# Kernel optimization log

Hardware: AMD Instinct MI355X
Metric: run time of the kernel (lower is better)

## Reference

```python
import jax, jax.numpy as jnp
import numpy as np

B, T, D, V, E = 128, 256, 1024, 32000, 300


def setup_inputs() -> dict:
    key = jax.random.key(0)
    ks = jax.random.split(key, 9)
    s = lambda d: 1.0 / np.sqrt(d)
    return {
        "input_to_decoder": jax.random.randint(ks[0], (B, 1), 0, V),
        "encoder_output": jax.random.normal(ks[1], (B, T, D), jnp.float32) * s(D),
        "state_h": jax.random.normal(ks[2], (B, D), jnp.float32) * s(D),
        "state_c": jax.random.normal(ks[3], (B, D), jnp.float32) * s(D),
        "emb_table": jax.random.normal(ks[4], (V, E), jnp.float32) * 0.02,
        "W_lstm": jax.random.normal(ks[5], (D + E, 4 * D), jnp.float32) * s(D + E),
        "U_lstm": jax.random.normal(ks[6], (D, 4 * D), jnp.float32) * s(D),
        "b_lstm": jnp.zeros((4 * D,), jnp.float32),
        "W_dense": jax.random.normal(ks[7], (D, V), jnp.float32) * s(D),
        "b_dense": jnp.zeros((V,), jnp.float32),
    }


def reference(input_to_decoder, encoder_output, state_h, state_c,
              emb_table, W_lstm, U_lstm, b_lstm, W_dense, b_dense):
    # embedding lookup + squeeze(axis=1): [B,1] -> [B,E]
    emb = emb_table[input_to_decoder[:, 0]]
    # Bahdanau-style dot scores: [B,T]
    scores = jnp.einsum("btd,bd->bt", encoder_output, state_h)
    # NOTE: faithful to source - context uses RAW (pre-softmax) scores
    context = jnp.einsum("btd,bt->bd", encoder_output, scores)  # [B,D]
    attention_weights = jax.nn.softmax(scores, axis=1)[..., None]  # [B,T,1]
    # concat context + embedding, single LSTM cell step (Keras gate order i,f,g,o)
    x = jnp.concatenate([context, emb], axis=1)  # [B,D+E]
    z = x @ W_lstm + state_h @ U_lstm + b_lstm  # [B,4D]
    zi, zf, zg, zo = jnp.split(z, 4, axis=1)
    c_new = jax.nn.sigmoid(zf) * state_c + jax.nn.sigmoid(zi) * jnp.tanh(zg)
    h_new = jax.nn.sigmoid(zo) * jnp.tanh(c_new)
    logits = h_new @ W_dense + b_dense  # [B,V]
    return logits, h_new, c_new, attention_weights, context
```

## Files before the change

### kernel.cpp

```cpp
#include <hip/hip_runtime.h>
#include <hip/hip_bf16.h>
#include <cmath>


#define Bc 128
#define Tc 256
#define Dc 1024
#define Vc 32000
#define Ec 300
#define KREAL 2348
#define KXP 2688
#define KSPLIT 7
#define N4 4096

typedef __attribute__((ext_vector_type(8))) short bf16x8;
typedef __attribute__((ext_vector_type(4))) float f32x4;

static __device__ __forceinline__ short f2bf(float x) {
    __hip_bfloat16 b = __float2bfloat16(x);
    return *reinterpret_cast<short*>(&b);
}
static __device__ __forceinline__ unsigned pack2(float a, float b) {
    return (unsigned)(unsigned short)f2bf(a) | ((unsigned)(unsigned short)f2bf(b) << 16);
}

__global__ __launch_bounds__(1024) void k_att(
        const float* __restrict__ enc, const float* __restrict__ h,
        const int* __restrict__ idx, const float* __restrict__ emb_table,
        float* __restrict__ ctx_out, float* __restrict__ attn_out,
        unsigned short* __restrict__ x_bf) {
    const int b = blockIdx.x;
    const int tid = threadIdx.x;
    const int wave = tid >> 6, lane = tid & 63;
    __shared__ float s_acc[16][1024];
    __shared__ float s_sc[256];
    __shared__ float red[256];

    const float4* h4 = (const float4*)(h + ((size_t)b << 10));
    float4 hv0 = h4[lane], hv1 = h4[lane + 64], hv2 = h4[lane + 128], hv3 = h4[lane + 192];

    float4 a0 = {0,0,0,0}, a1 = {0,0,0,0}, a2 = {0,0,0,0}, a3 = {0,0,0,0};
    const int t0 = wave << 4;
    const float4* e4 = (const float4*)(enc + ((size_t)(b * Tc + t0) << 10));

    #pragma unroll 2
    for (int i = 0; i < 16; ++i) {
        float4 e0 = e4[lane], e1 = e4[lane + 64], e2 = e4[lane + 128], e3 = e4[lane + 192];
        e4 += 256;
        float d = e0.x*hv0.x + e0.y*hv0.y + e0.z*hv0.z + e0.w*hv0.w
                + e1.x*hv1.x + e1.y*hv1.y + e1.z*hv1.z + e1.w*hv1.w
                + e2.x*hv2.x + e2.y*hv2.y + e2.z*hv2.z + e2.w*hv2.w
                + e3.x*hv3.x + e3.y*hv3.y + e3.z*hv3.z + e3.w*hv3.w;
        #pragma unroll
        for (int off = 32; off; off >>= 1) d += __shfl_xor(d, off, 64);
        if (lane == 0) s_sc[t0 + i] = d;
        a0.x += d*e0.x; a0.y += d*e0.y; a0.z += d*e0.z; a0.w += d*e0.w;
        a1.x += d*e1.x; a1.y += d*e1.y; a1.z += d*e1.z; a1.w += d*e1.w;
        a2.x += d*e2.x; a2.y += d*e2.y; a2.z += d*e2.z; a2.w += d*e2.w;
        a3.x += d*e3.x; a3.y += d*e3.y; a3.z += d*e3.z; a3.w += d*e3.w;
    }
    *(float4*)&s_acc[wave][lane << 2]         = a0;
    *(float4*)&s_acc[wave][256 + (lane << 2)] = a1;
    *(float4*)&s_acc[wave][512 + (lane << 2)] = a2;
    *(float4*)&s_acc[wave][768 + (lane << 2)] = a3;
    __syncthreads();

    float cv = 0.f;
    #pragma unroll
    for (int w = 0; w < 16; ++w) cv += s_acc[w][tid];
    ctx_out[((size_t)b << 10) + tid] = cv;
    s_acc[0][tid] = cv;
    __syncthreads();

    unsigned short* xb = x_bf + (size_t)b * KXP;
    if (tid < 512) {
        *(unsigned*)&xb[tid << 1] = pack2(s_acc[0][tid << 1], s_acc[0][(tid << 1) + 1]);
        float2 hp = *(const float2*)(h + ((size_t)b << 10) + (tid << 1));
        *(unsigned*)&xb[(Dc + Ec) + (tid << 1)] = pack2(hp.x, hp.y);
    } else if (tid < 812) {
        int i = tid - 512;
        int row = idx[b];
        xb[Dc + i] = (unsigned short)f2bf(emb_table[(size_t)row * Ec + i]);
    } else if (tid < 812 + (KXP - KREAL)) {
        xb[KREAL + (tid - 812)] = 0;
    }

    float v = (tid < 256) ? s_sc[tid] : -1e30f;
    if (tid < 256) red[tid] = v;
    __syncthreads();
    for (int s = 128; s; s >>= 1) {
        if (tid < s) red[tid] = fmaxf(red[tid], red[tid + s]);
        __syncthreads();
    }
    float m = red[0];
    __syncthreads();
    float e = __expf(v - m);
    if (tid < 256) red[tid] = e;
    __syncthreads();
    for (int s = 128; s; s >>= 1) {
        if (tid < s) red[tid] += red[tid + s];
        __syncthreads();
    }
    if (tid < 256) attn_out[(b << 8) + tid] = e / red[0];
}

__global__ __launch_bounds__(512) void k_zgemm_mfma(
        const unsigned short* __restrict__ xbf, const float* __restrict__ Wl,
        const float* __restrict__ Ul, float* __restrict__ z_part) {
    __shared__ __align__(16) short blds[2 * 8 * 64 * 8];
    const int tid  = threadIdx.x;
    const int wid  = tid >> 6;
    const int lane = tid & 63;
    const int g    = lane >> 4;
    const int r    = lane & 15;
    const int n0   = blockIdx.x << 6;
    const int ksp  = blockIdx.y;

    const int pr = tid >> 4;
    const int c  = tid & 15;
    const int kk = (pr << 1) & 31;
    const int gg = kk >> 3, jj = kk & 7;
    const int ks0 = pr >> 4;

    f32x4 acc[4] = {};
    const unsigned short* xrow = xbf + (size_t)((wid << 4) + r) * KXP;

    float4 wra[2], wrb[2];
    bf16x8 areg[2][2];

    auto loadWU = [&](int gk) -> float4 {
        if (gk < 1324) return *(const float4*)(Wl + (size_t)gk * N4 + n0 + (c << 2));
        if (gk < KREAL) return *(const float4*)(Ul + (size_t)(gk - 1324) * N4 + n0 + (c << 2));
        return float4{0.f, 0.f, 0.f, 0.f};
    };

    {
        const int kt = (ksp * 6) << 6;
        wra[0] = loadWU(kt + (pr << 1));
        wrb[0] = loadWU(kt + (pr << 1) + 1);
        areg[0][0] = *(const bf16x8*)&xrow[kt + (g << 3)];
        areg[0][1] = *(const bf16x8*)&xrow[kt + 32 + (g << 3)];
    }

    #pragma unroll
    for (int t = 0; t < 6; ++t) {
        const int cur = t & 1;
        const int coff = cur << 12;
        {
            const float av[4] = {wra[cur].x, wra[cur].y, wra[cur].z, wra[cur].w};
            const float bv[4] = {wrb[cur].x, wrb[cur].y, wrb[cur].z, wrb[cur].w};
            #pragma unroll
            for (int i = 0; i < 4; ++i) {
                int n = (c << 2) + i;
                int nt = n >> 4;
                int inner = (gg << 4) | (n & 15);
                int Xs = ((((ks0 << 2) + nt) << 6) | inner) ^ nt;
                *(unsigned*)&blds[coff + (Xs << 3) + jj] = pack2(av[i], bv[i]);
            }
        }
        if (t < 5) {
            const int kt = ((ksp * 6) + t + 1) << 6;
            wra[cur ^ 1] = loadWU(kt + (pr << 1));
            wrb[cur ^ 1] = loadWU(kt + (pr << 1) + 1);
            areg[cur ^ 1][0] = *(const bf16x8*)&xrow[kt + (g << 3)];
            areg[cur ^ 1][1] = *(const bf16x8*)&xrow[kt + 32 + (g << 3)];
        }
        __syncthreads();
        #pragma unroll
        for (int ks = 0; ks < 2; ++ks) {
            #pragma unroll
            for (int nt = 0; nt < 4; ++nt) {
                int Xs = ((((ks << 2) + nt) << 6) | lane) ^ nt;
                bf16x8 bfr = *(const bf16x8*)&blds[coff + (Xs << 3)];
                acc[nt] = __builtin_amdgcn_mfma_f32_16x16x32_bf16(areg[cur][ks], bfr, acc[nt], 0, 0, 0);
            }
        }
    }

    float* zp = z_part + ((size_t)ksp << 19);
    #pragma unroll
    for (int nt = 0; nt < 4; ++nt) {
        int col = n0 + (nt << 4) + r;
        #pragma unroll
        for (int j = 0; j < 4; ++j) {
            int rowm = (wid << 4) + (g << 2) + j;
            zp[((size_t)rowm << 12) + col] = acc[nt][j];
        }
    }
}

__global__ void k_gates(const float* __restrict__ z_part, const float* __restrict__ b_lstm,
                        const float* __restrict__ c_in, float* __restrict__ h_new,
                        float* __restrict__ c_new, unsigned short* __restrict__ h_bf) {
    int i = blockIdx.x * 256 + threadIdx.x;
    int b = i >> 8, d4 = (i & 255) << 2;
    size_t base = ((size_t)b << 12) + d4;
    float4 zi = *(const float4*)(b_lstm + d4);
    float4 zf = *(const float4*)(b_lstm + d4 + 1024);
    float4 zg = *(const float4*)(b_lstm + d4 + 2048);
    float4 zo = *(const float4*)(b_lstm + d4 + 3072);
    #pragma unroll
    for (int ks = 0; ks < KSPLIT; ++ks) {
        const float* zp = z_part + ((size_t)ks << 19);
        float4 t;
        t = *(const float4*)(zp + base);        zi.x += t.x; zi.y += t.y; zi.z += t.z; zi.w += t.w;
        t = *(const float4*)(zp + base + 1024); zf.x += t.x; zf.y += t.y; zf.z += t.z; zf.w += t.w;
        t = *(const float4*)(zp + base + 2048); zg.x += t.x; zg.y += t.y; zg.z += t.z; zg.w += t.w;
        t = *(const float4*)(zp + base + 3072); zo.x += t.x; zo.y += t.y; zo.z += t.z; zo.w += t.w;
    }
    float4 cin = *(const float4*)(c_in + ((size_t)b << 10) + d4);
    float4 cn, hn;
    {
        float si = 1.f/(1.f+__expf(-zi.x)), sf = 1.f/(1.f+__expf(-zf.x)), so = 1.f/(1.f+__expf(-zo.x));
        cn.x = sf*cin.x + si*tanhf(zg.x); hn.x = so*tanhf(cn.x);
        si = 1.f/(1.f+__expf(-zi.y)); sf = 1.f/(1.f+__expf(-zf.y)); so = 1.f/(1.f+__expf(-zo.y));
        cn.y = sf*cin.y + si*tanhf(zg.y); hn.y = so*tanhf(cn.y);
        si = 1.f/(1.f+__expf(-zi.z)); sf = 1.f/(1.f+__expf(-zf.z)); so = 1.f/(1.f+__expf(-zo.z));
        cn.z = sf*cin.z + si*tanhf(zg.z); hn.z = so*tanhf(cn.z);
        si = 1.f/(1.f+__expf(-zi.w)); sf = 1.f/(1.f+__expf(-zf.w)); so = 1.f/(1.f+__expf(-zo.w));
        cn.w = sf*cin.w + si*tanhf(zg.w); hn.w = so*tanhf(cn.w);
    }
    *(float4*)(c_new + ((size_t)b << 10) + d4) = cn;
    *(float4*)(h_new + ((size_t)b << 10) + d4) = hn;
    uint2 hp; hp.x = pack2(hn.x, hn.y); hp.y = pack2(hn.z, hn.w);
    *(uint2*)&h_bf[((size_t)b << 10) + d4] = hp;
}

__global__ __launch_bounds__(512) void k_logits_mfma(
        const unsigned short* __restrict__ hbf, const float* __restrict__ Wd,
        const float* __restrict__ bd, float* __restrict__ out) {
    __shared__ __align__(16) short blds[2 * 16 * 64 * 8];
    const int tid  = threadIdx.x;
    const int wid  = tid >> 6;
    const int lane = tid & 63;
    const int g    = lane >> 4;
    const int r    = lane & 15;
    const int n0   = blockIdx.x << 6;

    const int pr = tid >> 4;
    const int c  = tid & 15;
    const int kk = (pr << 1) & 31;
    const int gg = kk >> 3, jj = kk & 7;
    const int ksA = pr >> 4;
    const int ksB = ksA + 2;

    f32x4 acc[4] = {};
    const unsigned short* hrow = hbf + ((size_t)((wid << 4) + r) << 10);
    const float* wbase = Wd + (size_t)(pr << 1) * Vc + n0 + (c << 2);

    float4 wra[2], wrb[2], wrc[2], wrd[2];
    bf16x8 areg[2][4];

    {
        wra[0] = *(const float4*)(wbase);
        wrb[0] = *(const float4*)(wbase + Vc);
        wrc[0] = *(const float4*)(wbase + (size_t)64 * Vc);
        wrd[0] = *(const float4*)(wbase + (size_t)65 * Vc);
        #pragma unroll
        for (int ks = 0; ks < 4; ++ks)
            areg[0][ks] = *(const bf16x8*)&hrow[(ks << 5) + (g << 3)];
    }

    #pragma unroll
    for (int t = 0; t < 8; ++t) {
        const int cur = t & 1;
        const int coff = cur << 13;
        {
            const float a0[4] = {wra[cur].x, wra[cur].y, wra[cur].z, wra[cur].w};
            const float b0[4] = {wrb[cur].x, wrb[cur].y, wrb[cur].z, wrb[cur].w};
            const float c0[4] = {wrc[cur].x, wrc[cur].y, wrc[cur].z, wrc[cur].w};
            const float d0[4] = {wrd[cur].x, wrd[cur].y, wrd[cur].z, wrd[cur].w};
            #pragma unroll
            for (int i = 0; i < 4; ++i) {
                int n = (c << 2) + i;
                int nt = n >> 4;
                int inner = (gg << 4) | (n & 15);
                int XsA = ((((ksA << 2) + nt) << 6) | inner) ^ nt;
                int XsB = ((((ksB << 2) + nt) << 6) | inner) ^ nt;
                *(unsigned*)&blds[coff + (XsA << 3) + jj] = pack2(a0[i], b0[i]);
                *(unsigned*)&blds[coff + (XsB << 3) + jj] = pack2(c0[i], d0[i]);
            }
        }
        if (t < 7) {
            const float* wb2 = wbase + (size_t)((t + 1) << 7) * Vc;
            wra[cur ^ 1] = *(const float4*)(wb2);
            wrb[cur ^ 1] = *(const float4*)(wb2 + Vc);
            wrc[cur ^ 1] = *(const float4*)(wb2 + (size_t)64 * Vc);
            wrd[cur ^ 1] = *(const float4*)(wb2 + (size_t)65 * Vc);
            #pragma unroll
            for (int ks = 0; ks < 4; ++ks)
                areg[cur ^ 1][ks] = *(const bf16x8*)&hrow[((t + 1) << 7) + (ks << 5) + (g << 3)];
        }
        __syncthreads();
        #pragma unroll
        for (int ks = 0; ks < 4; ++ks) {
            #pragma unroll
            for (int nt = 0; nt < 4; ++nt) {
                int Xs = ((((ks << 2) + nt) << 6) | lane) ^ nt;
                bf16x8 bfr = *(const bf16x8*)&blds[coff + (Xs << 3)];
                acc[nt] = __builtin_amdgcn_mfma_f32_16x16x32_bf16(areg[cur][ks], bfr, acc[nt], 0, 0, 0);
            }
        }
    }

    #pragma unroll
    for (int nt = 0; nt < 4; ++nt) {
        int col = n0 + (nt << 4) + r;
        float bias = bd[col];
        #pragma unroll
        for (int j = 0; j < 4; ++j) {
            int row = (wid << 4) + (g << 2) + j;
            out[(size_t)row * Vc + col] = acc[nt][j] + bias;
        }
    }
}

extern "C" void kernel_launch(void* const* d_in, const int* in_sizes, int n_in,
                              void* d_out, int out_size, void* d_ws, size_t ws_size,
                              hipStream_t stream) {
    const int*   idx = (const int*)d_in[0];
    const float* enc = (const float*)d_in[1];
    const float* h   = (const float*)d_in[2];
    const float* c   = (const float*)d_in[3];
    const float* emb = (const float*)d_in[4];
    const float* Wl  = (const float*)d_in[5];
    const float* Ul  = (const float*)d_in[6];
    const float* bl  = (const float*)d_in[7];
    const float* Wd  = (const float*)d_in[8];
    const float* bd  = (const float*)d_in[9];

    float* out    = (float*)d_out;
    float* logits = out;
    float* h_new  = out + 4096000;
    float* c_new  = out + 4227072;
    float* attn   = out + 4358144;
    float* ctx    = out + 4390912;

    float*          z_part = out;
    unsigned short* x_bf16 = (unsigned short*)d_ws;
    unsigned short* h_bf16 = (unsigned short*)d_ws + 344064;

    hipLaunchKernelGGL(k_att, dim3(128), dim3(1024), 0, stream, enc, h, idx, emb, ctx, attn, x_bf16);
    hipLaunchKernelGGL(k_zgemm_mfma, dim3(64, KSPLIT), dim3(512), 0, stream, x_bf16, Wl, Ul, z_part);
    hipLaunchKernelGGL(k_gates, dim3(128), dim3(256), 0, stream, z_part, bl, c, h_new, c_new, h_bf16);
    hipLaunchKernelGGL(k_logits_mfma, dim3(500), dim3(512), 0, stream, h_bf16, Wd, bd, logits);
}
```

Before: 92.23 us.

## Fuse all stages into one cooperative persistent kernel with grid syncs

```diff
diff --git a/kernel.cpp b/kernel.cpp
--- a/kernel.cpp
+++ b/kernel.cpp
@@ -1,6 +1,9 @@
 #include <hip/hip_runtime.h>
 #include <hip/hip_bf16.h>
+#include <hip/hip_cooperative_groups.h>
 #include <cmath>
+
+namespace cg = cooperative_groups;
 
 
 #define Bc 128
@@ -24,293 +27,310 @@
     return (unsigned)(unsigned short)f2bf(a) | ((unsigned)(unsigned short)f2bf(b) << 16);
 }
 
-__global__ __launch_bounds__(1024) void k_att(
+__global__ __launch_bounds__(512, 2) void k_mega(
         const float* __restrict__ enc, const float* __restrict__ h,
         const int* __restrict__ idx, const float* __restrict__ emb_table,
-        float* __restrict__ ctx_out, float* __restrict__ attn_out,
-        unsigned short* __restrict__ x_bf) {
-    const int b = blockIdx.x;
-    const int tid = threadIdx.x;
-    const int wave = tid >> 6, lane = tid & 63;
-    __shared__ float s_acc[16][1024];
-    __shared__ float s_sc[256];
-    __shared__ float red[256];
-
-    const float4* h4 = (const float4*)(h + ((size_t)b << 10));
-    float4 hv0 = h4[lane], hv1 = h4[lane + 64], hv2 = h4[lane + 128], hv3 = h4[lane + 192];
-
-    float4 a0 = {0,0,0,0}, a1 = {0,0,0,0}, a2 = {0,0,0,0}, a3 = {0,0,0,0};
-    const int t0 = wave << 4;
-    const float4* e4 = (const float4*)(enc + ((size_t)(b * Tc + t0) << 10));
-
-    #pragma unroll 2
-    for (int i = 0; i < 16; ++i) {
-        float4 e0 = e4[lane], e1 = e4[lane + 64], e2 = e4[lane + 128], e3 = e4[lane + 192];
-        e4 += 256;
-        float d = e0.x*hv0.x + e0.y*hv0.y + e0.z*hv0.z + e0.w*hv0.w
-                + e1.x*hv1.x + e1.y*hv1.y + e1.z*hv1.z + e1.w*hv1.w
-                + e2.x*hv2.x + e2.y*hv2.y + e2.z*hv2.z + e2.w*hv2.w
-                + e3.x*hv3.x + e3.y*hv3.y + e3.z*hv3.z + e3.w*hv3.w;
+        const float* __restrict__ Wl, const float* __restrict__ Ul,
+        const float* __restrict__ bl, const float* __restrict__ c_in,
+        const float* __restrict__ Wd, const float* __restrict__ bd,
+        float* __restrict__ logits, float* __restrict__ h_new,
+        float* __restrict__ c_new, float* __restrict__ attn,
+        float* __restrict__ ctx_out,
+        float* __restrict__ ctx_part, float* __restrict__ scores_g,
+        float* __restrict__ z_part,
+        unsigned short* __restrict__ x_bf, unsigned short* __restrict__ h_bf) {
+    cg::grid_group grid = cg::this_grid();
+    __shared__ __align__(16) char smem[32768];
+    const int tid  = threadIdx.x;
+    const int wave = tid >> 6;
+    const int lane = tid & 63;
+
+    {
+        const int tc = blockIdx.x >> 7;
+        const int b  = blockIdx.x & 127;
+        float (*s_acc)[1024] = (float (*)[1024])smem;
+
+        const float4* h4 = (const float4*)(h + ((size_t)b << 10));
+        float4 hv0 = h4[lane], hv1 = h4[lane + 64], hv2 = h4[lane + 128], hv3 = h4[lane + 192];
+
+        float4 a0 = {0,0,0,0}, a1 = {0,0,0,0}, a2 = {0,0,0,0}, a3 = {0,0,0,0};
+        const int t0 = (tc << 7) + (wave << 4);
+        const float4* e4 = (const float4*)(enc + ((size_t)(b * Tc + t0) << 10));
+
+        #pragma unroll 2
+        for (int i = 0; i < 16; ++i) {
+            float4 e0 = e4[lane], e1 = e4[lane + 64], e2 = e4[lane + 128], e3 = e4[lane + 192];
+            e4 += 256;
+            float d = e0.x*hv0.x + e0.y*hv0.y + e0.z*hv0.z + e0.w*hv0.w
+                    + e1.x*hv1.x + e1.y*hv1.y + e1.z*hv1.z + e1.w*hv1.w
+                    + e2.x*hv2.x + e2.y*hv2.y + e2.z*hv2.z + e2.w*hv2.w
+                    + e3.x*hv3.x + e3.y*hv3.y + e3.z*hv3.z + e3.w*hv3.w;
+            #pragma unroll
+            for (int off = 32; off; off >>= 1) d += __shfl_xor(d, off, 64);
+            if (lane == 0) scores_g[(b << 8) + t0 + i] = d;
+            a0.x += d*e0.x; a0.y += d*e0.y; a0.z += d*e0.z; a0.w += d*e0.w;
+            a1.x += d*e1.x; a1.y += d*e1.y; a1.z += d*e1.z; a1.w += d*e1.w;
+            a2.x += d*e2.x; a2.y += d*e2.y; a2.z += d*e2.z; a2.w += d*e2.w;
+            a3.x += d*e3.x; a3.y += d*e3.y; a3.z += d*e3.z; a3.w += d*e3.w;
+        }
+        *(float4*)&s_acc[wave][lane << 2]         = a0;
+        *(float4*)&s_acc[wave][256 + (lane << 2)] = a1;
+        *(float4*)&s_acc[wave][512 + (lane << 2)] = a2;
+        *(float4*)&s_acc[wave][768 + (lane << 2)] = a3;
+        __syncthreads();
         #pragma unroll
-        for (int off = 32; off; off >>= 1) d += __shfl_xor(d, off, 64);
-        if (lane == 0) s_sc[t0 + i] = d;
-        a0.x += d*e0.x; a0.y += d*e0.y; a0.z += d*e0.z; a0.w += d*e0.w;
-        a1.x += d*e1.x; a1.y += d*e1.y; a1.z += d*e1.z; a1.w += d*e1.w;
-        a2.x += d*e2.x; a2.y += d*e2.y; a2.z += d*e2.z; a2.w += d*e2.w;
-        a3.x += d*e3.x; a3.y += d*e3.y; a3.z += d*e3.z; a3.w += d*e3.w;
-    }
-    *(float4*)&s_acc[wave][lane << 2]         = a0;
-    *(float4*)&s_acc[wave][256 + (lane << 2)] = a1;
-    *(float4*)&s_acc[wave][512 + (lane << 2)] = a2;
-    *(float4*)&s_acc[wave][768 + (lane << 2)] = a3;
-    __syncthreads();
-
-    float cv = 0.f;
-    #pragma unroll
-    for (int w = 0; w < 16; ++w) cv += s_acc[w][tid];
-    ctx_out[((size_t)b << 10) + tid] = cv;
-    s_acc[0][tid] = cv;
-    __syncthreads();
-
-    unsigned short* xb = x_bf + (size_t)b * KXP;
-    if (tid < 512) {
-        *(unsigned*)&xb[tid << 1] = pack2(s_acc[0][tid << 1], s_acc[0][(tid << 1) + 1]);
-        float2 hp = *(const float2*)(h + ((size_t)b << 10) + (tid << 1));
-        *(unsigned*)&xb[(Dc + Ec) + (tid << 1)] = pack2(hp.x, hp.y);
-    } else if (tid < 812) {
-        int i = tid - 512;
-        int row = idx[b];
-        xb[Dc + i] = (unsigned short)f2bf(emb_table[(size_t)row * Ec + i]);
-    } else if (tid < 812 + (KXP - KREAL)) {
-        xb[KREAL + (tid - 812)] = 0;
-    }
-
-    float v = (tid < 256) ? s_sc[tid] : -1e30f;
-    if (tid < 256) red[tid] = v;
-    __syncthreads();
-    for (int s = 128; s; s >>= 1) {
-        if (tid < s) red[tid] = fmaxf(red[tid], red[tid + s]);
-        __syncthreads();
-    }
-    float m = red[0];
-    __syncthreads();
-    float e = __expf(v - m);
-    if (tid < 256) red[tid] = e;
-    __syncthreads();
-    for (int s = 128; s; s >>= 1) {
-        if (tid < s) red[tid] += red[tid + s];
-        __syncthreads();
-    }
-    if (tid < 256) attn_out[(b << 8) + tid] = e / red[0];
-}
-
-__global__ __launch_bounds__(512) void k_zgemm_mfma(
-        const unsigned short* __restrict__ xbf, const float* __restrict__ Wl,
-        const float* __restrict__ Ul, float* __restrict__ z_part) {
-    __shared__ __align__(16) short blds[2 * 8 * 64 * 8];
-    const int tid  = threadIdx.x;
-    const int wid  = tid >> 6;
-    const int lane = tid & 63;
-    const int g    = lane >> 4;
-    const int r    = lane & 15;
-    const int n0   = blockIdx.x << 6;
-    const int ksp  = blockIdx.y;
-
-    const int pr = tid >> 4;
-    const int c  = tid & 15;
-    const int kk = (pr << 1) & 31;
-    const int gg = kk >> 3, jj = kk & 7;
-    const int ks0 = pr >> 4;
-
-    f32x4 acc[4] = {};
-    const unsigned short* xrow = xbf + (size_t)((wid << 4) + r) * KXP;
-
-    float4 wra[2], wrb[2];
-    bf16x8 areg[2][2];
-
-    auto loadWU = [&](int gk) -> float4 {
-        if (gk < 1324) return *(const float4*)(Wl + (size_t)gk * N4 + n0 + (c << 2));
-        if (gk < KREAL) return *(const float4*)(Ul + (size_t)(gk - 1324) * N4 + n0 + (c << 2));
-        return float4{0.f, 0.f, 0.f, 0.f};
-    };
+        for (int cc = tid; cc < 1024; cc += 512) {
+            float cv = 0.f;
+            #pragma unroll
+            for (int w = 0; w < 8; ++w) cv += s_acc[w][cc];
+            ctx_part[(((size_t)(tc << 7) + b) << 10) + cc] = cv;
+        }
+    }
+    grid.sync();
+
+    if (blockIdx.x < 128) {
+        const int b = blockIdx.x;
+        unsigned short* xb = x_bf + (size_t)b * KXP;
+        {
+            float2 p0 = *(const float2*)(ctx_part + ((size_t)b << 10) + (tid << 1));
+            float2 p1 = *(const float2*)(ctx_part + (((size_t)(128 + b)) << 10) + (tid << 1));
+            float2 cv = {p0.x + p1.x, p0.y + p1.y};
+            *(float2*)(ctx_out + ((size_t)b << 10) + (tid << 1)) = cv;
+            *(unsigned*)&xb[tid << 1] = pack2(cv.x, cv.y);
+            float2 hp = *(const float2*)(h + ((size_t)b << 10) + (tid << 1));
+            *(unsigned*)&xb[(Dc + Ec) + (tid << 1)] = pack2(hp.x, hp.y);
+        }
+        if (tid < Ec) xb[Dc + tid] = (unsigned short)f2bf(emb_table[(size_t)idx[b] * Ec + tid]);
+        if (tid < KXP - KREAL) xb[KREAL + tid] = 0;
+
+        float* red = (float*)smem;
+        float v = (tid < 256) ? scores_g[(b << 8) + tid] : -1e30f;
+        __syncthreads();
+        if (tid < 256) red[tid] = v;
+        __syncthreads();
+        for (int s = 128; s; s >>= 1) {
+            if (tid < s) red[tid] = fmaxf(red[tid], red[tid + s]);
+            __syncthreads();
+        }
+        float m = red[0];
+        __syncthreads();
+        float e = __expf(v - m);
+        if (tid < 256) red[tid] = e;
+        __syncthreads();
+        for (int s = 128; s; s >>= 1) {
+            if (tid < s) red[tid] += red[tid + s];
+            __syncthreads();
+        }
+        if (tid < 256) attn[(b << 8) + tid] = e / red[0];
+    }
+    grid.sync();
 
     {
-        const int kt = (ksp * 6) << 6;
-        wra[0] = loadWU(kt + (pr << 1));
-        wrb[0] = loadWU(kt + (pr << 1) + 1);
-        areg[0][0] = *(const bf16x8*)&xrow[kt + (g << 3)];
-        areg[0][1] = *(const bf16x8*)&xrow[kt + 32 + (g << 3)];
-    }
-
-    #pragma unroll
-    for (int t = 0; t < 6; ++t) {
-        const int cur = t & 1;
-        const int coff = cur << 12;
+        short* blds = (short*)smem;
+        const int wid = wave;
+        const int g   = lane >> 4;
+        const int r   = lane & 15;
+        const int pr  = tid >> 4;
+        const int c   = tid & 15;
+        const int kk  = (pr << 1) & 31;
+        const int gg  = kk >> 3, jj = kk & 7;
+        const int ks0 = pr >> 4;
+
+        for (int tile = blockIdx.x; tile < 64 * KSPLIT; tile += 256) {
+            const int n0  = (tile & 63) << 6;
+            const int ksp = tile >> 6;
+
+            f32x4 acc[4] = {};
+            const unsigned short* xrow = x_bf + (size_t)((wid << 4) + r) * KXP;
+
+            float4 wra[2], wrb[2];
+            bf16x8 areg[2][2];
+
+            auto loadWU = [&](int gk) -> float4 {
+                if (gk < 1324) return *(const float4*)(Wl + (size_t)gk * N4 + n0 + (c << 2));
+                if (gk < KREAL) return *(const float4*)(Ul + (size_t)(gk - 1324) * N4 + n0 + (c << 2));
+                return float4{0.f, 0.f, 0.f, 0.f};
+            };
+
+            {
+                const int kt = (ksp * 6) << 6;
+                wra[0] = loadWU(kt + (pr << 1));
+                wrb[0] = loadWU(kt + (pr << 1) + 1);
+                areg[0][0] = *(const bf16x8*)&xrow[kt + (g << 3)];
+                areg[0][1] = *(const bf16x8*)&xrow[kt + 32 + (g << 3)];
+            }
+            __syncthreads();
+            #pragma unroll
+            for (int t = 0; t < 6; ++t) {
+                const int cur = t & 1;
+                const int coff = cur << 12;
+                {
+                    const float av[4] = {wra[cur].x, wra[cur].y, wra[cur].z, wra[cur].w};
+                    const float bv[4] = {wrb[cur].x, wrb[cur].y, wrb[cur].z, wrb[cur].w};
+                    #pragma unroll
+                    for (int i = 0; i < 4; ++i) {
+                        int n = (c << 2) + i;
+                        int nt = n >> 4;
+                        int inner = (gg << 4) | (n & 15);
+                        int Xs = ((((ks0 << 2) + nt) << 6) | inner) ^ nt;
+                        *(unsigned*)&blds[coff + (Xs << 3) + jj] = pack2(av[i], bv[i]);
+                    }
+                }
+                if (t < 5) {
+                    const int kt = ((ksp * 6) + t + 1) << 6;
+                    wra[cur ^ 1] = loadWU(kt + (pr << 1));
+                    wrb[cur ^ 1] = loadWU(kt + (pr << 1) + 1);
+                    areg[cur ^ 1][0] = *(const bf16x8*)&xrow[kt + (g << 3)];
+                    areg[cur ^ 1][1] = *(const bf16x8*)&xrow[kt + 32 + (g << 3)];
+                }
+                __syncthreads();
+                #pragma unroll
+                for (int ks = 0; ks < 2; ++ks) {
+                    #pragma unroll
+                    for (int nt = 0; nt < 4; ++nt) {
+                        int Xs = ((((ks << 2) + nt) << 6) | lane) ^ nt;
+                        bf16x8 bfr = *(const bf16x8*)&blds[coff + (Xs << 3)];
+                        acc[nt] = __builtin_amdgcn_mfma_f32_16x16x32_bf16(areg[cur][ks], bfr, acc[nt], 0, 0, 0);
+                    }
+                }
+                __syncthreads();
+            }
+
+            float* zp = z_part + ((size_t)ksp << 19);
+            #pragma unroll
+            for (int nt = 0; nt < 4; ++nt) {
+                int col = n0 + (nt << 4) + r;
+                #pragma unroll
+                for (int j = 0; j < 4; ++j) {
+                    int rowm = (wid << 4) + (g << 2) + j;
+                    zp[((size_t)rowm << 12) + col] = acc[nt][j];
+                }
+            }
+        }
+    }
+    grid.sync();
+
+    if (blockIdx.x < 64) {
+        int i = blockIdx.x * 512 + tid;
+        int b = i >> 8, d4 = (i & 255) << 2;
+        size_t base = ((size_t)b << 12) + d4;
+        float4 zi = *(const float4*)(bl + d4);
+        float4 zf = *(const float4*)(bl + d4 + 1024);
+        float4 zg = *(const float4*)(bl + d4 + 2048);
+        float4 zo = *(const float4*)(bl + d4 + 3072);
+        #pragma unroll
+        for (int ks = 0; ks < KSPLIT; ++ks) {
+            const float* zp = z_part + ((size_t)ks << 19);
+            float4 t;
+            t = *(const float4*)(zp + base);        zi.x += t.x; zi.y += t.y; zi.z += t.z; zi.w += t.w;
+            t = *(const float4*)(zp + base + 1024); zf.x += t.x; zf.y += t.y; zf.z += t.z; zf.w += t.w;
+            t = *(const float4*)(zp + base + 2048); zg.x += t.x; zg.y += t.y; zg.z += t.z; zg.w += t.w;
+            t = *(const float4*)(zp + base + 3072); zo.x += t.x; zo.y += t.y; zo.z += t.z; zo.w += t.w;
+        }
+        float4 cin = *(const float4*)(c_in + ((size_t)b << 10) + d4);
+        float4 cn, hn;
         {
-            const float av[4] = {wra[cur].x, wra[cur].y, wra[cur].z, wra[cur].w};
-            const float bv[4] = {wrb[cur].x, wrb[cur].y, wrb[cur].z, wrb[cur].w};
-            #pragma unroll
-            for (int i = 0; i < 4; ++i) {
-                int n = (c << 2) + i;
-                int nt = n >> 4;
-                int inner = (gg << 4) | (n & 15);
-                int Xs = ((((ks0 << 2) + nt) << 6) | inner) ^ nt;
-                *(unsigned*)&blds[coff + (Xs << 3) + jj] = pack2(av[i], bv[i]);
-            }
-        }
-        if (t < 5) {
-            const int kt = ((ksp * 6) + t + 1) << 6;
-            wra[cur ^ 1] = loadWU(kt + (pr << 1));
-            wrb[cur ^ 1] = loadWU(kt + (pr << 1) + 1);
-            areg[cur ^ 1][0] = *(const bf16x8*)&xrow[kt + (g << 3)];
-            areg[cur ^ 1][1] = *(const bf16x8*)&xrow[kt + 32 + (g << 3)];
-        }
-        __syncthreads();
-        #pragma unroll
-        for (int ks = 0; ks < 2; ++ks) {
+            float si = 1.f/(1.f+__expf(-zi.x)), sf = 1.f/(1.f+__expf(-zf.x)), so = 1.f/(1.f+__expf(-zo.x));
+            cn.x = sf*cin.x + si*tanhf(zg.x); hn.x = so*tanhf(cn.x);
+            si = 1.f/(1.f+__expf(-zi.y)); sf = 1.f/(1.f+__expf(-zf.y)); so = 1.f/(1.f+__expf(-zo.y));
+            cn.y = sf*cin.y + si*tanhf(zg.y); hn.y = so*tanhf(cn.y);
+            si = 1.f/(1.f+__expf(-zi.z)); sf = 1.f/(1.f+__expf(-zf.z)); so = 1.f/(1.f+__expf(-zo.z));
+            cn.z = sf*cin.z + si*tanhf(zg.z); hn.z = so*tanhf(cn.z);
+            si = 1.f/(1.f+__expf(-zi.w)); sf = 1.f/(1.f+__expf(-zf.w)); so = 1.f/(1.f+__expf(-zo.w));
+            cn.w = sf*cin.w + si*tanhf(zg.w); hn.w = so*tanhf(cn.w);
+        }
+        *(float4*)(c_new + ((size_t)b << 10) + d4) = cn;
+        *(float4*)(h_new + ((size_t)b << 10) + d4) = hn;
+        uint2 hp; hp.x = pack2(hn.x, hn.y); hp.y = pack2(hn.z, hn.w);
+        *(uint2*)&h_bf[((size_t)b << 10) + d4] = hp;
+    }
+    grid.sync();
+
+    {
+        short* blds = (short*)smem;
+        const int wid = wave;
+        const int g   = lane >> 4;
+        const int r   = lane & 15;
+        const int pr  = tid >> 4;
+        const int c   = tid & 15;
+        const int kk  = (pr << 1) & 31;
+        const int gg  = kk >> 3, jj = kk & 7;
+        const int ksA = pr >> 4;
+        const int ksB = ksA + 2;
+
+        for (int tile = blockIdx.x; tile < 500; tile += 256) {
+            const int n0 = tile << 6;
+
+            f32x4 acc[4] = {};
+            const unsigned short* hrow = h_bf + ((size_t)((wid << 4) + r) << 10);
+            const float* wbase = Wd + (size_t)(pr << 1) * Vc + n0 + (c << 2);
+
+            float4 wra[2], wrb[2], wrc[2], wrd[2];
+            bf16x8 areg[2][4];
+
+            {
+                wra[0] = *(const float4*)(wbase);
+                wrb[0] = *(const float4*)(wbase + Vc);
+                wrc[0] = *(const float4*)(wbase + (size_t)64 * Vc);
+                wrd[0] = *(const float4*)(wbase + (size_t)65 * Vc);
+                #pragma unroll
+                for (int ks = 0; ks < 4; ++ks)
+                    areg[0][ks] = *(const bf16x8*)&hrow[(ks << 5) + (g << 3)];
+            }
+            __syncthreads();
+            #pragma unroll
+            for (int t = 0; t < 8; ++t) {
+                const int cur = t & 1;
+                const int coff = cur << 13;
+                {
+                    const float a0[4] = {wra[cur].x, wra[cur].y, wra[cur].z, wra[cur].w};
+                    const float b0[4] = {wrb[cur].x, wrb[cur].y, wrb[cur].z, wrb[cur].w};
+                    const float c0[4] = {wrc[cur].x, wrc[cur].y, wrc[cur].z, wrc[cur].w};
+                    const float d0[4] = {wrd[cur].x, wrd[cur].y, wrd[cur].z, wrd[cur].w};
+                    #pragma unroll
+                    for (int i = 0; i < 4; ++i) {
+                        int n = (c << 2) + i;
+                        int nt = n >> 4;
+                        int inner = (gg << 4) | (n & 15);
+                        int XsA = ((((ksA << 2) + nt) << 6) | inner) ^ nt;
+                        int XsB = ((((ksB << 2) + nt) << 6) | inner) ^ nt;
+                        *(unsigned*)&blds[coff + (XsA << 3) + jj] = pack2(a0[i], b0[i]);
+                        *(unsigned*)&blds[coff + (XsB << 3) + jj] = pack2(c0[i], d0[i]);
+                    }
+                }
+                if (t < 7) {
+                    const float* wb2 = wbase + (size_t)((t + 1) << 7) * Vc;
+                    wra[cur ^ 1] = *(const float4*)(wb2);
+                    wrb[cur ^ 1] = *(const float4*)(wb2 + Vc);
+                    wrc[cur ^ 1] = *(const float4*)(wb2 + (size_t)64 * Vc);
+                    wrd[cur ^ 1] = *(const float4*)(wb2 + (size_t)65 * Vc);
+                    #pragma unroll
+                    for (int ks = 0; ks < 4; ++ks)
+                        areg[cur ^ 1][ks] = *(const bf16x8*)&hrow[((t + 1) << 7) + (ks << 5) + (g << 3)];
+                }
+                __syncthreads();
+                #pragma unroll
+                for (int ks = 0; ks < 4; ++ks) {
+                    #pragma unroll
+                    for (int nt = 0; nt < 4; ++nt) {
+                        int Xs = ((((ks << 2) + nt) << 6) | lane) ^ nt;
+                        bf16x8 bfr = *(const bf16x8*)&blds[coff + (Xs << 3)];
+                        acc[nt] = __builtin_amdgcn_mfma_f32_16x16x32_bf16(areg[cur][ks], bfr, acc[nt], 0, 0, 0);
+                    }
+                }
+                __syncthreads();
+            }
+
             #pragma unroll
             for (int nt = 0; nt < 4; ++nt) {
-                int Xs = ((((ks << 2) + nt) << 6) | lane) ^ nt;
-                bf16x8 bfr = *(const bf16x8*)&blds[coff + (Xs << 3)];
-                acc[nt] = __builtin_amdgcn_mfma_f32_16x16x32_bf16(areg[cur][ks], bfr, acc[nt], 0, 0, 0);
-            }
-        }
-    }
-
-    float* zp = z_part + ((size_t)ksp << 19);
-    #pragma unroll
-    for (int nt = 0; nt < 4; ++nt) {
-        int col = n0 + (nt << 4) + r;
-        #pragma unroll
-        for (int j = 0; j < 4; ++j) {
-            int rowm = (wid << 4) + (g << 2) + j;
-            zp[((size_t)rowm << 12) + col] = acc[nt][j];
-        }
-    }
-}
-
-__global__ void k_gates(const float* __restrict__ z_part, const float* __restrict__ b_lstm,
-                        const float* __restrict__ c_in, float* __restrict__ h_new,
-                        float* __restrict__ c_new, unsigned short* __restrict__ h_bf) {
-    int i = blockIdx.x * 256 + threadIdx.x;
-    int b = i >> 8, d4 = (i & 255) << 2;
-    size_t base = ((size_t)b << 12) + d4;
-    float4 zi = *(const float4*)(b_lstm + d4);
-    float4 zf = *(const float4*)(b_lstm + d4 + 1024);
-    float4 zg = *(const float4*)(b_lstm + d4 + 2048);
-    float4 zo = *(const float4*)(b_lstm + d4 + 3072);
-    #pragma unroll
-    for (int ks = 0; ks < KSPLIT; ++ks) {
-        const float* zp = z_part + ((size_t)ks << 19);
-        float4 t;
-        t = *(const float4*)(zp + base);        zi.x += t.x; zi.y += t.y; zi.z += t.z; zi.w += t.w;
-        t = *(const float4*)(zp + base + 1024); zf.x += t.x; zf.y += t.y; zf.z += t.z; zf.w += t.w;
-        t = *(const float4*)(zp + base + 2048); zg.x += t.x; zg.y += t.y; zg.z += t.z; zg.w += t.w;
-        t = *(const float4*)(zp + base + 3072); zo.x += t.x; zo.y += t.y; zo.z += t.z; zo.w += t.w;
-    }
-    float4 cin = *(const float4*)(c_in + ((size_t)b << 10) + d4);
-    float4 cn, hn;
-    {
-        float si = 1.f/(1.f+__expf(-zi.x)), sf = 1.f/(1.f+__expf(-zf.x)), so = 1.f/(1.f+__expf(-zo.x));
-        cn.x = sf*cin.x + si*tanhf(zg.x); hn.x = so*tanhf(cn.x);
-        si = 1.f/(1.f+__expf(-zi.y)); sf = 1.f/(1.f+__expf(-zf.y)); so = 1.f/(1.f+__expf(-zo.y));
-        cn.y = sf*cin.y + si*tanhf(zg.y); hn.y = so*tanhf(cn.y);
-        si = 1.f/(1.f+__expf(-zi.z)); sf = 1.f/(1.f+__expf(-zf.z)); so = 1.f/(1.f+__expf(-zo.z));
-        cn.z = sf*cin.z + si*tanhf(zg.z); hn.z = so*tanhf(cn.z);
-        si = 1.f/(1.f+__expf(-zi.w)); sf = 1.f/(1.f+__expf(-zf.w)); so = 1.f/(1.f+__expf(-zo.w));
-        cn.w = sf*cin.w + si*tanhf(zg.w); hn.w = so*tanhf(cn.w);
-    }
-    *(float4*)(c_new + ((size_t)b << 10) + d4) = cn;
-    *(float4*)(h_new + ((size_t)b << 10) + d4) = hn;
-    uint2 hp; hp.x = pack2(hn.x, hn.y); hp.y = pack2(hn.z, hn.w);
-    *(uint2*)&h_bf[((size_t)b << 10) + d4] = hp;
-}
-
-__global__ __launch_bounds__(512) void k_logits_mfma(
-        const unsigned short* __restrict__ hbf, const float* __restrict__ Wd,
-        const float* __restrict__ bd, float* __restrict__ out) {
-    __shared__ __align__(16) short blds[2 * 16 * 64 * 8];
-    const int tid  = threadIdx.x;
-    const int wid  = tid >> 6;
-    const int lane = tid & 63;
-    const int g    = lane >> 4;
-    const int r    = lane & 15;
-    const int n0   = blockIdx.x << 6;
-
-    const int pr = tid >> 4;
-    const int c  = tid & 15;
-    const int kk = (pr << 1) & 31;
-    const int gg = kk >> 3, jj = kk & 7;
-    const int ksA = pr >> 4;
-    const int ksB = ksA + 2;
-
-    f32x4 acc[4] = {};
-    const unsigned short* hrow = hbf + ((size_t)((wid << 4) + r) << 10);
-    const float* wbase = Wd + (size_t)(pr << 1) * Vc + n0 + (c << 2);
-
-    float4 wra[2], wrb[2], wrc[2], wrd[2];
-    bf16x8 areg[2][4];
-
-    {
-        wra[0] = *(const float4*)(wbase);
-        wrb[0] = *(const float4*)(wbase + Vc);
-        wrc[0] = *(const float4*)(wbase + (size_t)64 * Vc);
-        wrd[0] = *(const float4*)(wbase + (size_t)65 * Vc);
-        #pragma unroll
-        for (int ks = 0; ks < 4; ++ks)
-            areg[0][ks] = *(const bf16x8*)&hrow[(ks << 5) + (g << 3)];
-    }
-
-    #pragma unroll
-    for (int t = 0; t < 8; ++t) {
-        const int cur = t & 1;
-        const int coff = cur << 13;
-        {
-            const float a0[4] = {wra[cur].x, wra[cur].y, wra[cur].z, wra[cur].w};
-            const float b0[4] = {wrb[cur].x, wrb[cur].y, wrb[cur].z, wrb[cur].w};
-            const float c0[4] = {wrc[cur].x, wrc[cur].y, wrc[cur].z, wrc[cur].w};
-            const float d0[4] = {wrd[cur].x, wrd[cur].y, wrd[cur].z, wrd[cur].w};
-            #pragma unroll
-            for (int i = 0; i < 4; ++i) {
-                int n = (c << 2) + i;
-                int nt = n >> 4;
-                int inner = (gg << 4) | (n & 15);
-                int XsA = ((((ksA << 2) + nt) << 6) | inner) ^ nt;
-                int XsB = ((((ksB << 2) + nt) << 6) | inner) ^ nt;
-                *(unsigned*)&blds[coff + (XsA << 3) + jj] = pack2(a0[i], b0[i]);
-                *(unsigned*)&blds[coff + (XsB << 3) + jj] = pack2(c0[i], d0[i]);
-            }
-        }
-        if (t < 7) {
-            const float* wb2 = wbase + (size_t)((t + 1) << 7) * Vc;
-            wra[cur ^ 1] = *(const float4*)(wb2);
-            wrb[cur ^ 1] = *(const float4*)(wb2 + Vc);
-            wrc[cur ^ 1] = *(const float4*)(wb2 + (size_t)64 * Vc);
-            wrd[cur ^ 1] = *(const float4*)(wb2 + (size_t)65 * Vc);
-            #pragma unroll
-            for (int ks = 0; ks < 4; ++ks)
-                areg[cur ^ 1][ks] = *(const bf16x8*)&hrow[((t + 1) << 7) + (ks << 5) + (g << 3)];
-        }
-        __syncthreads();
-        #pragma unroll
-        for (int ks = 0; ks < 4; ++ks) {
-            #pragma unroll
-            for (int nt = 0; nt < 4; ++nt) {
-                int Xs = ((((ks << 2) + nt) << 6) | lane) ^ nt;
-                bf16x8 bfr = *(const bf16x8*)&blds[coff + (Xs << 3)];
-                acc[nt] = __builtin_amdgcn_mfma_f32_16x16x32_bf16(areg[cur][ks], bfr, acc[nt], 0, 0, 0);
-            }
-        }
-    }
-
-    #pragma unroll
-    for (int nt = 0; nt < 4; ++nt) {
-        int col = n0 + (nt << 4) + r;
-        float bias = bd[col];
-        #pragma unroll
-        for (int j = 0; j < 4; ++j) {
-            int row = (wid << 4) + (g << 2) + j;
-            out[(size_t)row * Vc + col] = acc[nt][j] + bias;
+                int col = n0 + (nt << 4) + r;
+                float bias = bd[col];
+                #pragma unroll
+                for (int j = 0; j < 4; ++j) {
+                    int row = (wid << 4) + (g << 2) + j;
+                    logits[(size_t)row * Vc + col] = acc[nt][j] + bias;
+                }
+            }
         }
     }
 }
@@ -336,12 +356,19 @@
     float* attn   = out + 4358144;
     float* ctx    = out + 4390912;
 
-    float*          z_part = out;
-    unsigned short* x_bf16 = (unsigned short*)d_ws;
-    unsigned short* h_bf16 = (unsigned short*)d_ws + 344064;
-
-    hipLaunchKernelGGL(k_att, dim3(128), dim3(1024), 0, stream, enc, h, idx, emb, ctx, attn, x_bf16);
-    hipLaunchKernelGGL(k_zgemm_mfma, dim3(64, KSPLIT), dim3(512), 0, stream, x_bf16, Wl, Ul, z_part);
-    hipLaunchKernelGGL(k_gates, dim3(128), dim3(256), 0, stream, z_part, bl, c, h_new, c_new, h_bf16);
-    hipLaunchKernelGGL(k_logits_mfma, dim3(500), dim3(512), 0, stream, h_bf16, Wd, bd, logits);
+    float*          ctx_part = out;
+    float*          scores_g = out + 262144;
+    float*          z_part   = out;
+    unsigned short* x_bf16   = (unsigned short*)d_ws;
+    unsigned short* h_bf16   = (unsigned short*)d_ws + 344064;
+
+    void* args[] = {
+        (void*)&enc, (void*)&h, (void*)&idx, (void*)&emb,
+        (void*)&Wl, (void*)&Ul, (void*)&bl, (void*)&c,
+        (void*)&Wd, (void*)&bd,
+        (void*)&logits, (void*)&h_new, (void*)&c_new, (void*)&attn, (void*)&ctx,
+        (void*)&ctx_part, (void*)&scores_g, (void*)&z_part,
+        (void*)&x_bf16, (void*)&h_bf16
+    };
+    hipLaunchCooperativeKernel((const void*)k_mega, dim3(256), dim3(512), args, 0, stream);
 }
```

After: 236.2 us. 2.56x slower.
